# Kernel optimization log

Hardware: AMD Instinct MI355X
Metric: run time of the kernel (lower is better)

The kernel has to match this reference:

```python
import jax, jax.numpy as jnp
import numpy as np

SIZE = 65536
MAX_EDGES = 16777216  # n_edges = min(0.1*SIZE^2, MAX_EDGES) = MAX_EDGES, so all edges active


def setup_inputs() -> dict:
    key = jax.random.key(0)
    k1, k2, k3, k4 = jax.random.split(key, 4)
    x = jax.random.normal(k1, (SIZE,), dtype=jnp.float32)
    edge_weights = jax.random.normal(k2, (MAX_EDGES,), dtype=jnp.float32) * (2.0 / SIZE) ** 0.5
    bias = jnp.zeros((SIZE,), dtype=jnp.float32)
    src = jax.random.randint(k3, (MAX_EDGES,), 0, SIZE, dtype=jnp.int64 if jax.config.jax_enable_x64 else jnp.int32)
    dst = jax.random.randint(k4, (MAX_EDGES,), 0, SIZE, dtype=jnp.int64 if jax.config.jax_enable_x64 else jnp.int32)
    return {"x": x, "edge_weights": edge_weights, "bias": bias, "src": src, "dst": dst}


def reference(x, edge_weights, bias, src, dst):
    # gather -> elementwise multiply -> scatter_add -> + bias
    weighted = x[src] * edge_weights                    # [E]
    out = jax.ops.segment_sum(weighted, dst, num_segments=SIZE)  # [size]
    return out + bias
```

## Files before the change

kernel.cpp:

```cpp
#include <hip/hip_runtime.h>


#define NNODES  65536
#define NEDGES  16777216
#define THREADS 1024
#define NCOPIES 128
#define GROUPS  16
#define CPG     (NCOPIES / GROUPS)
#define RANGES  2
#define BINS    (NNODES / RANGES)

#define FIXSCALE   4194304.0f
#define FIXINV     (1.0f / 4194304.0f)

template <bool HALF>
__global__ __launch_bounds__(THREADS, 4) void wx_lds_kernel(
    const float* __restrict__ x,
    const float* __restrict__ w,
    const int*   __restrict__ src,
    void*        __restrict__ wxv)
{
    extern __shared__ _Float16 xs[];

    for (int i = threadIdx.x; i < NNODES / 4; i += THREADS) {
        float4 v = ((const float4*)x)[i];
        union { _Float16 hh[4]; short4 s4; } u;
        u.hh[0] = (_Float16)v.x; u.hh[1] = (_Float16)v.y;
        u.hh[2] = (_Float16)v.z; u.hh[3] = (_Float16)v.w;
        ((short4*)xs)[i] = u.s4;
    }
    __syncthreads();

    const int n8 = NEDGES / 8;
    const int gs = gridDim.x * THREADS;
    for (int i = blockIdx.x * THREADS + (int)threadIdx.x; i < n8; i += gs) {
        int4   s0 = ((const int4*)src)[2 * i];
        int4   s1 = ((const int4*)src)[2 * i + 1];
        float4 w0 = ((const float4*)w)[2 * i];
        float4 w1 = ((const float4*)w)[2 * i + 1];

        float v[8] = {
            (float)xs[s0.x] * w0.x, (float)xs[s0.y] * w0.y,
            (float)xs[s0.z] * w0.z, (float)xs[s0.w] * w0.w,
            (float)xs[s1.x] * w1.x, (float)xs[s1.y] * w1.y,
            (float)xs[s1.z] * w1.z, (float)xs[s1.w] * w1.w };

        if constexpr (HALF) {
            union { _Float16 hh[8]; int4 p; } u;
            #pragma unroll
            for (int k = 0; k < 8; ++k) u.hh[k] = (_Float16)v[k];
            ((int4*)wxv)[i] = u.p;
        } else {
            float4 o0 = { v[0], v[1], v[2], v[3] };
            float4 o1 = { v[4], v[5], v[6], v[7] };
            ((float4*)wxv)[2 * i]     = o0;
            ((float4*)wxv)[2 * i + 1] = o1;
        }
    }
}

template <bool HALF>
__global__ __launch_bounds__(THREADS, 4) void hist2_kernel(
    const int*  __restrict__ dst,
    const void* __restrict__ wxv,
    float*      __restrict__ ws,
    int B)
{
    extern __shared__ int hi[];

    const int b = blockIdx.x;
    int r, c;
    if (B == NCOPIES) {
        r = (b >> 3) & (RANGES - 1);
        c = (b & 7) | ((b >> 4) << 3);
    } else {
        r = b & (RANGES - 1);
        c = b >> 1;
    }
    const int lo = r * BINS;

    for (int i = threadIdx.x; i < BINS; i += THREADS) hi[i] = 0;
    __syncthreads();

    const int4* dst4 = (const int4*)dst;
    const int n8     = NEDGES / 8;
    const int stride = B * THREADS;
    int g = c * THREADS + (int)threadIdx.x;

    if ((n8 % (2 * stride)) == 0 && n8 >= 2 * stride) {
        const int niter2 = n8 / (2 * stride);
        for (int it = 0; it < niter2; ++it, g += 2 * stride) {
            const int ga = g;
            const int gb = g + stride;

            int4 dA0 = dst4[2 * ga], dA1 = dst4[2 * ga + 1];
            int4 dB0 = dst4[2 * gb], dB1 = dst4[2 * gb + 1];

            float vv[16];
            if constexpr (HALF) {
                int4 pa = ((const int4*)wxv)[ga];
                int4 pb = ((const int4*)wxv)[gb];
                union { int4 p; _Float16 hh[8]; } ua, ub;
                ua.p = pa; ub.p = pb;
                #pragma unroll
                for (int k = 0; k < 8; ++k) {
                    vv[k]     = (float)ua.hh[k];
                    vv[8 + k] = (float)ub.hh[k];
                }
            } else {
                const float4* wx4 = (const float4*)wxv;
                float4 wA0 = wx4[2 * ga], wA1 = wx4[2 * ga + 1];
                float4 wB0 = wx4[2 * gb], wB1 = wx4[2 * gb + 1];
                vv[0]=wA0.x;  vv[1]=wA0.y;  vv[2]=wA0.z;  vv[3]=wA0.w;
                vv[4]=wA1.x;  vv[5]=wA1.y;  vv[6]=wA1.z;  vv[7]=wA1.w;
                vv[8]=wB0.x;  vv[9]=wB0.y;  vv[10]=wB0.z; vv[11]=wB0.w;
                vv[12]=wB1.x; vv[13]=wB1.y; vv[14]=wB1.z; vv[15]=wB1.w;
            }

            unsigned bin[16] = {
                (unsigned)(dA0.x - lo), (unsigned)(dA0.y - lo),
                (unsigned)(dA0.z - lo), (unsigned)(dA0.w - lo),
                (unsigned)(dA1.x - lo), (unsigned)(dA1.y - lo),
                (unsigned)(dA1.z - lo), (unsigned)(dA1.w - lo),
                (unsigned)(dB0.x - lo), (unsigned)(dB0.y - lo),
                (unsigned)(dB0.z - lo), (unsigned)(dB0.w - lo),
                (unsigned)(dB1.x - lo), (unsigned)(dB1.y - lo),
                (unsigned)(dB1.z - lo), (unsigned)(dB1.w - lo) };

            #pragma unroll
            for (int k = 0; k < 16; ++k) {
                if (bin[k] < (unsigned)BINS) {
                    int iv = __float2int_rn(vv[k] * FIXSCALE);
                    atomicAdd(&hi[bin[k]], iv);
                }
            }
        }
    } else {
        for (; g < n8; g += stride) {
            int4 d0 = dst4[2 * g], d1 = dst4[2 * g + 1];
            float vv[8];
            if constexpr (HALF) {
                int4 p = ((const int4*)wxv)[g];
                union { int4 p; _Float16 hh[8]; } u; u.p = p;
                #pragma unroll
                for (int k = 0; k < 8; ++k) vv[k] = (float)u.hh[k];
            } else {
                const float4* wx4 = (const float4*)wxv;
                float4 a = wx4[2 * g], bb = wx4[2 * g + 1];
                vv[0]=a.x; vv[1]=a.y; vv[2]=a.z; vv[3]=a.w;
                vv[4]=bb.x; vv[5]=bb.y; vv[6]=bb.z; vv[7]=bb.w;
            }
            unsigned bin[8] = {
                (unsigned)(d0.x - lo), (unsigned)(d0.y - lo),
                (unsigned)(d0.z - lo), (unsigned)(d0.w - lo),
                (unsigned)(d1.x - lo), (unsigned)(d1.y - lo),
                (unsigned)(d1.z - lo), (unsigned)(d1.w - lo) };
            #pragma unroll
            for (int k = 0; k < 8; ++k) {
                if (bin[k] < (unsigned)BINS) {
                    int iv = __float2int_rn(vv[k] * FIXSCALE);
                    atomicAdd(&hi[bin[k]], iv);
                }
            }
        }
    }
    __syncthreads();

    float* outc = ws + (size_t)c * NNODES + lo;
    for (int i = threadIdx.x; i < BINS; i += THREADS)
        outc[i] = (float)hi[i] * FIXINV;
}

__global__ __launch_bounds__(THREADS, 4) void hist_kernel(
    const float* __restrict__ x,
    const float* __restrict__ w,
    const int*   __restrict__ src,
    const int*   __restrict__ dst,
    float*       __restrict__ ws,
    int B)
{
    extern __shared__ float h[];

    const int b = blockIdx.x;
    int r, c;
    if (B == NCOPIES) {
        r = (b >> 3) & (RANGES - 1);
        c = (b & 7) | ((b >> 4) << 3);
    } else {
        r = b & (RANGES - 1);
        c = b >> 1;
    }
    const int lo = r * BINS;

    for (int i = threadIdx.x; i < BINS; i += THREADS) h[i] = 0.0f;
    __syncthreads();

    const int4*   src4 = (const int4*)src;
    const int4*   dst4 = (const int4*)dst;
    const float4* wgt4 = (const float4*)w;

    const int n8     = NEDGES / 8;
    const int stride = B * THREADS;
    int g = c * THREADS + (int)threadIdx.x;

    if ((n8 % (2 * stride)) == 0 && n8 >= 2 * stride) {
        const int niter2 = n8 / (2 * stride);
        for (int it = 0; it < niter2; ++it, g += 2 * stride) {
            const int ga = g;
            const int gb = g + stride;

            int4   sA0 = src4[2 * ga], sA1 = src4[2 * ga + 1];
            int4   sB0 = src4[2 * gb], sB1 = src4[2 * gb + 1];
            int4   dA0 = dst4[2 * ga], dA1 = dst4[2 * ga + 1];
            int4   dB0 = dst4[2 * gb], dB1 = dst4[2 * gb + 1];
            float4 wA0 = wgt4[2 * ga], wA1 = wgt4[2 * ga + 1];
            float4 wB0 = wgt4[2 * gb], wB1 = wgt4[2 * gb + 1];

            int s[16] = { sA0.x, sA0.y, sA0.z, sA0.w,
                          sA1.x, sA1.y, sA1.z, sA1.w,
                          sB0.x, sB0.y, sB0.z, sB0.w,
                          sB1.x, sB1.y, sB1.z, sB1.w };
            unsigned bin[16] = {
                (unsigned)(dA0.x - lo), (unsigned)(dA0.y - lo),
                (unsigned)(dA0.z - lo), (unsigned)(dA0.w - lo),
                (unsigned)(dA1.x - lo), (unsigned)(dA1.y - lo),
                (unsigned)(dA1.z - lo), (unsigned)(dA1.w - lo),
                (unsigned)(dB0.x - lo), (unsigned)(dB0.y - lo),
                (unsigned)(dB0.z - lo), (unsigned)(dB0.w - lo),
                (unsigned)(dB1.x - lo), (unsigned)(dB1.y - lo),
                (unsigned)(dB1.z - lo), (unsigned)(dB1.w - lo) };
            float wv[16] = { wA0.x, wA0.y, wA0.z, wA0.w,
                             wA1.x, wA1.y, wA1.z, wA1.w,
                             wB0.x, wB0.y, wB0.z, wB0.w,
                             wB1.x, wB1.y, wB1.z, wB1.w };

            float v[16];
            #pragma unroll
            for (int k = 0; k < 16; ++k) {
                v[k] = 0.0f;
                if (bin[k] < (unsigned)BINS) v[k] = x[s[k]] * wv[k];
            }
            #pragma unroll
            for (int k = 0; k < 16; ++k) {
                if (bin[k] < (unsigned)BINS) atomicAdd(&h[bin[k]], v[k]);
            }
        }
    } else {
        for (; g < n8; g += stride) {
            int4   sa = src4[2 * g], sb = src4[2 * g + 1];
            int4   da = dst4[2 * g], db = dst4[2 * g + 1];
            float4 wa = wgt4[2 * g], wb = wgt4[2 * g + 1];

            int      s[8]  = { sa.x, sa.y, sa.z, sa.w, sb.x, sb.y, sb.z, sb.w };
            unsigned bin[8] = {
                (unsigned)(da.x - lo), (unsigned)(da.y - lo),
                (unsigned)(da.z - lo), (unsigned)(da.w - lo),
                (unsigned)(db.x - lo), (unsigned)(db.y - lo),
                (unsigned)(db.z - lo), (unsigned)(db.w - lo) };
            float    wv[8] = { wa.x, wa.y, wa.z, wa.w, wb.x, wb.y, wb.z, wb.w };

            float v[8];
            #pragma unroll
            for (int k = 0; k < 8; ++k) {
                v[k] = 0.0f;
                if (bin[k] < (unsigned)BINS) v[k] = x[s[k]] * wv[k];
            }
            #pragma unroll
            for (int k = 0; k < 8; ++k) {
                if (bin[k] < (unsigned)BINS) atomicAdd(&h[bin[k]], v[k]);
            }
        }
    }
    __syncthreads();

    float* outc = ws + (size_t)c * NNODES + lo;
    for (int i = threadIdx.x; i < BINS; i += THREADS) outc[i] = h[i];
}

__global__ __launch_bounds__(256) void reduceA_kernel(float* __restrict__ ws)
{
    const int NB = NNODES / (256 * 4);
    int g  = blockIdx.x / NB;
    int jb = blockIdx.x % NB;
    int i4 = jb * 256 + (int)threadIdx.x;

    float4* w4 = (float4*)ws;
    const int stride4 = NNODES / 4;

    float4 acc = w4[(size_t)(g * CPG) * stride4 + i4];
    #pragma unroll
    for (int cc = 1; cc < CPG; ++cc) {
        float4 t = w4[(size_t)(g * CPG + cc) * stride4 + i4];
        acc.x += t.x; acc.y += t.y; acc.z += t.z; acc.w += t.w;
    }
    w4[(size_t)(g * CPG) * stride4 + i4] = acc;
}

__global__ __launch_bounds__(256) void reduceB_kernel(
    const float* __restrict__ ws,
    const float* __restrict__ bias,
    float*       __restrict__ out)
{
    int i4 = blockIdx.x * 256 + (int)threadIdx.x;
    const float4* w4 = (const float4*)ws;
    const int stride4 = NNODES / 4;

    float4 acc = ((const float4*)bias)[i4];
    #pragma unroll
    for (int g = 0; g < GROUPS; ++g) {
        float4 t = w4[(size_t)(g * CPG) * stride4 + i4];
        acc.x += t.x; acc.y += t.y; acc.z += t.z; acc.w += t.w;
    }
    ((float4*)out)[i4] = acc;
}

__global__ __launch_bounds__(256) void reduce_generic_kernel(
    const float* __restrict__ ws,
    const float* __restrict__ bias,
    float*       __restrict__ out,
    int B)
{
    int i = blockIdx.x * 256 + (int)threadIdx.x;
    float acc = bias[i];
    for (int cc = 0; cc < B; ++cc) acc += ws[(size_t)cc * NNODES + i];
    out[i] = acc;
}

__global__ __launch_bounds__(256) void init_out_kernel(
    const float* __restrict__ bias, float* __restrict__ out)
{
    int i = blockIdx.x * blockDim.x + threadIdx.x;
    if (i < NNODES) out[i] = bias[i];
}

__global__ __launch_bounds__(256) void edge_atomic_kernel(
    const float* __restrict__ x, const float* __restrict__ w,
    const int* __restrict__ src, const int* __restrict__ dst,
    float* __restrict__ out)
{
    const int n4 = NEDGES / 4;
    int tid = blockIdx.x * blockDim.x + threadIdx.x;
    int stride = gridDim.x * blockDim.x;
    for (int i = tid; i < n4; i += stride) {
        int4 s = ((const int4*)src)[i];
        int4 d = ((const int4*)dst)[i];
        float4 ww = ((const float4*)w)[i];
        atomicAdd(&out[d.x], x[s.x] * ww.x);
        atomicAdd(&out[d.y], x[s.y] * ww.y);
        atomicAdd(&out[d.z], x[s.z] * ww.z);
        atomicAdd(&out[d.w], x[s.w] * ww.w);
    }
}

extern "C" void kernel_launch(void* const* d_in, const int* in_sizes, int n_in,
                              void* d_out, int out_size, void* d_ws, size_t ws_size,
                              hipStream_t stream) {
    const float* x    = (const float*)d_in[0];
    const float* w    = (const float*)d_in[1];
    const float* bias = (const float*)d_in[2];
    const int*   src  = (const int*)d_in[3];
    const int*   dst  = (const int*)d_in[4];
    float* out = (float*)d_out;
    float* ws  = (float*)d_ws;

    const size_t copiesBytes = (size_t)NCOPIES * NNODES * sizeof(float);
    const size_t xLds = (size_t)NNODES * sizeof(_Float16);

    if (ws_size >= copiesBytes + (size_t)NEDGES * sizeof(float)) {
        void* wx = (void*)((char*)d_ws + copiesBytes);
        wx_lds_kernel<false><<<256, THREADS, xLds, stream>>>(x, w, src, wx);
        hist2_kernel<false><<<NCOPIES * RANGES, THREADS,
                              BINS * sizeof(int), stream>>>(dst, wx, ws, NCOPIES);
        reduceA_kernel<<<GROUPS * (NNODES / 1024), 256, 0, stream>>>(ws);
        reduceB_kernel<<<NNODES / 1024, 256, 0, stream>>>(ws, bias, out);
    } else if (ws_size >= copiesBytes + (size_t)NEDGES * 2) {
        void* wx = (void*)((char*)d_ws + copiesBytes);
        wx_lds_kernel<true><<<256, THREADS, xLds, stream>>>(x, w, src, wx);
        hist2_kernel<true><<<NCOPIES * RANGES, THREADS,
                             BINS * sizeof(int), stream>>>(dst, wx, ws, NCOPIES);
        reduceA_kernel<<<GROUPS * (NNODES / 1024), 256, 0, stream>>>(ws);
        reduceB_kernel<<<NNODES / 1024, 256, 0, stream>>>(ws, bias, out);
    } else {
        size_t copies = ws_size / ((size_t)NNODES * sizeof(float));
        int B = (int)(copies < NCOPIES ? copies : NCOPIES);
        if (B >= 1) {
            hist_kernel<<<B * RANGES, THREADS, BINS * sizeof(float), stream>>>(
                x, w, src, dst, ws, B);
            if (B == NCOPIES) {
                reduceA_kernel<<<GROUPS * (NNODES / 1024), 256, 0, stream>>>(ws);
                reduceB_kernel<<<NNODES / 1024, 256, 0, stream>>>(ws, bias, out);
            } else {
                reduce_generic_kernel<<<NNODES / 256, 256, 0, stream>>>(ws, bias, out, B);
            }
        } else {
            init_out_kernel<<<NNODES / 256, 256, 0, stream>>>(bias, out);
            edge_atomic_kernel<<<4096, 256, 0, stream>>>(x, w, src, dst, out);
        }
    }
}
```

Before: 243.5 us.

## Always use half-precision intermediate products and software-prefetch edge loads in gather kernel

The launcher now always takes the fp16 path for the intermediate weighted-edge buffer, dropping the fp32 path even when workspace allows it. This halves that buffer's write and read traffic between the gather and histogram kernels. The gather kernel gains a register double-buffered loop that loads the next iteration's src and weight vectors before computing the current one. The fallback hist kernel loses its two-at-a-time unrolled loop for a plain loop. Rounding each product to fp16 adds precision error to the accumulated sums.

New measurement: 230.6 us. -5.3%, faster.

```diff
diff --git a/kernel.cpp b/kernel.cpp
--- a/kernel.cpp
+++ b/kernel.cpp
@@ -31,30 +31,82 @@
     }
     __syncthreads();
 
+    const int4*   src4 = (const int4*)src;
+    const float4* wgt4 = (const float4*)w;
+
     const int n8 = NEDGES / 8;
     const int gs = gridDim.x * THREADS;
-    for (int i = blockIdx.x * THREADS + (int)threadIdx.x; i < n8; i += gs) {
-        int4   s0 = ((const int4*)src)[2 * i];
-        int4   s1 = ((const int4*)src)[2 * i + 1];
-        float4 w0 = ((const float4*)w)[2 * i];
-        float4 w1 = ((const float4*)w)[2 * i + 1];
-
-        float v[8] = {
-            (float)xs[s0.x] * w0.x, (float)xs[s0.y] * w0.y,
-            (float)xs[s0.z] * w0.z, (float)xs[s0.w] * w0.w,
-            (float)xs[s1.x] * w1.x, (float)xs[s1.y] * w1.y,
-            (float)xs[s1.z] * w1.z, (float)xs[s1.w] * w1.w };
-
-        if constexpr (HALF) {
-            union { _Float16 hh[8]; int4 p; } u;
-            #pragma unroll
-            for (int k = 0; k < 8; ++k) u.hh[k] = (_Float16)v[k];
-            ((int4*)wxv)[i] = u.p;
-        } else {
-            float4 o0 = { v[0], v[1], v[2], v[3] };
-            float4 o1 = { v[4], v[5], v[6], v[7] };
-            ((float4*)wxv)[2 * i]     = o0;
-            ((float4*)wxv)[2 * i + 1] = o1;
+    int i = blockIdx.x * THREADS + (int)threadIdx.x;
+
+    if ((n8 % gs) == 0 && (n8 / gs) >= 2) {
+        const int niter = n8 / gs;
+        int4   s0 = src4[2 * i],  s1 = src4[2 * i + 1];
+        float4 w0 = wgt4[2 * i],  w1 = wgt4[2 * i + 1];
+
+        for (int it = 0; it < niter - 1; ++it) {
+            const int inext = i + gs;
+            int4   ns0 = src4[2 * inext], ns1 = src4[2 * inext + 1];
+            float4 nw0 = wgt4[2 * inext], nw1 = wgt4[2 * inext + 1];
+
+            float v[8] = {
+                (float)xs[s0.x] * w0.x, (float)xs[s0.y] * w0.y,
+                (float)xs[s0.z] * w0.z, (float)xs[s0.w] * w0.w,
+                (float)xs[s1.x] * w1.x, (float)xs[s1.y] * w1.y,
+                (float)xs[s1.z] * w1.z, (float)xs[s1.w] * w1.w };
+
+            if constexpr (HALF) {
+                union { _Float16 hh[8]; int4 p; } u;
+                #pragma unroll
+                for (int k = 0; k < 8; ++k) u.hh[k] = (_Float16)v[k];
+                ((int4*)wxv)[i] = u.p;
+            } else {
+                float4 o0 = { v[0], v[1], v[2], v[3] };
+                float4 o1 = { v[4], v[5], v[6], v[7] };
+                ((float4*)wxv)[2 * i]     = o0;
+                ((float4*)wxv)[2 * i + 1] = o1;
+            }
+
+            s0 = ns0; s1 = ns1; w0 = nw0; w1 = nw1;
+            i = inext;
+        }
+        {
+            float v[8] = {
+                (float)xs[s0.x] * w0.x, (float)xs[s0.y] * w0.y,
+                (float)xs[s0.z] * w0.z, (float)xs[s0.w] * w0.w,
+                (float)xs[s1.x] * w1.x, (float)xs[s1.y] * w1.y,
+                (float)xs[s1.z] * w1.z, (float)xs[s1.w] * w1.w };
+            if constexpr (HALF) {
+                union { _Float16 hh[8]; int4 p; } u;
+                #pragma unroll
+                for (int k = 0; k < 8; ++k) u.hh[k] = (_Float16)v[k];
+                ((int4*)wxv)[i] = u.p;
+            } else {
+                float4 o0 = { v[0], v[1], v[2], v[3] };
+                float4 o1 = { v[4], v[5], v[6], v[7] };
+                ((float4*)wxv)[2 * i]     = o0;
+                ((float4*)wxv)[2 * i + 1] = o1;
+            }
+        }
+    } else {
+        for (; i < n8; i += gs) {
+            int4   s0 = src4[2 * i], s1 = src4[2 * i + 1];
+            float4 w0 = wgt4[2 * i], w1 = wgt4[2 * i + 1];
+            float v[8] = {
+                (float)xs[s0.x] * w0.x, (float)xs[s0.y] * w0.y,
+                (float)xs[s0.z] * w0.z, (float)xs[s0.w] * w0.w,
+                (float)xs[s1.x] * w1.x, (float)xs[s1.y] * w1.y,
+                (float)xs[s1.z] * w1.z, (float)xs[s1.w] * w1.w };
+            if constexpr (HALF) {
+                union { _Float16 hh[8]; int4 p; } u;
+                #pragma unroll
+                for (int k = 0; k < 8; ++k) u.hh[k] = (_Float16)v[k];
+                ((int4*)wxv)[i] = u.p;
+            } else {
+                float4 o0 = { v[0], v[1], v[2], v[3] };
+                float4 o1 = { v[4], v[5], v[6], v[7] };
+                ((float4*)wxv)[2 * i]     = o0;
+                ((float4*)wxv)[2 * i + 1] = o1;
+            }
         }
     }
 }
@@ -203,72 +255,28 @@
     const int stride = B * THREADS;
     int g = c * THREADS + (int)threadIdx.x;
 
-    if ((n8 % (2 * stride)) == 0 && n8 >= 2 * stride) {
-        const int niter2 = n8 / (2 * stride);
-        for (int it = 0; it < niter2; ++it, g += 2 * stride) {
-            const int ga = g;
-            const int gb = g + stride;
-
-            int4   sA0 = src4[2 * ga], sA1 = src4[2 * ga + 1];
-            int4   sB0 = src4[2 * gb], sB1 = src4[2 * gb + 1];
-            int4   dA0 = dst4[2 * ga], dA1 = dst4[2 * ga + 1];
-            int4   dB0 = dst4[2 * gb], dB1 = dst4[2 * gb + 1];
-            float4 wA0 = wgt4[2 * ga], wA1 = wgt4[2 * ga + 1];
-            float4 wB0 = wgt4[2 * gb], wB1 = wgt4[2 * gb + 1];
-
-            int s[16] = { sA0.x, sA0.y, sA0.z, sA0.w,
-                          sA1.x, sA1.y, sA1.z, sA1.w,
-                          sB0.x, sB0.y, sB0.z, sB0.w,
-                          sB1.x, sB1.y, sB1.z, sB1.w };
-            unsigned bin[16] = {
-                (unsigned)(dA0.x - lo), (unsigned)(dA0.y - lo),
-                (unsigned)(dA0.z - lo), (unsigned)(dA0.w - lo),
-                (unsigned)(dA1.x - lo), (unsigned)(dA1.y - lo),
-                (unsigned)(dA1.z - lo), (unsigned)(dA1.w - lo),
-                (unsigned)(dB0.x - lo), (unsigned)(dB0.y - lo),
-                (unsigned)(dB0.z - lo), (unsigned)(dB0.w - lo),
-                (unsigned)(dB1.x - lo), (unsigned)(dB1.y - lo),
-                (unsigned)(dB1.z - lo), (unsigned)(dB1.w - lo) };
-            float wv[16] = { wA0.x, wA0.y, wA0.z, wA0.w,
-                             wA1.x, wA1.y, wA1.z, wA1.w,
-                             wB0.x, wB0.y, wB0.z, wB0.w,
-                             wB1.x, wB1.y, wB1.z, wB1.w };
-
-            float v[16];
-            #pragma unroll
-            for (int k = 0; k < 16; ++k) {
-                v[k] = 0.0f;
-                if (bin[k] < (unsigned)BINS) v[k] = x[s[k]] * wv[k];
-            }
-            #pragma unroll
-            for (int k = 0; k < 16; ++k) {
-                if (bin[k] < (unsigned)BINS) atomicAdd(&h[bin[k]], v[k]);
-            }
-        }
-    } else {
-        for (; g < n8; g += stride) {
-            int4   sa = src4[2 * g], sb = src4[2 * g + 1];
-            int4   da = dst4[2 * g], db = dst4[2 * g + 1];
-            float4 wa = wgt4[2 * g], wb = wgt4[2 * g + 1];
-
-            int      s[8]  = { sa.x, sa.y, sa.z, sa.w, sb.x, sb.y, sb.z, sb.w };
-            unsigned bin[8] = {
-                (unsigned)(da.x - lo), (unsigned)(da.y - lo),
-                (unsigned)(da.z - lo), (unsigned)(da.w - lo),
-                (unsigned)(db.x - lo), (unsigned)(db.y - lo),
-                (unsigned)(db.z - lo), (unsigned)(db.w - lo) };
-            float    wv[8] = { wa.x, wa.y, wa.z, wa.w, wb.x, wb.y, wb.z, wb.w };
-
-            float v[8];
-            #pragma unroll
-            for (int k = 0; k < 8; ++k) {
-                v[k] = 0.0f;
-                if (bin[k] < (unsigned)BINS) v[k] = x[s[k]] * wv[k];
-            }
-            #pragma unroll
-            for (int k = 0; k < 8; ++k) {
-                if (bin[k] < (unsigned)BINS) atomicAdd(&h[bin[k]], v[k]);
-            }
+    for (; g < n8; g += stride) {
+        int4   sa = src4[2 * g], sb = src4[2 * g + 1];
+        int4   da = dst4[2 * g], db = dst4[2 * g + 1];
+        float4 wa = wgt4[2 * g], wb = wgt4[2 * g + 1];
+
+        int      s[8]  = { sa.x, sa.y, sa.z, sa.w, sb.x, sb.y, sb.z, sb.w };
+        unsigned bin[8] = {
+            (unsigned)(da.x - lo), (unsigned)(da.y - lo),
+            (unsigned)(da.z - lo), (unsigned)(da.w - lo),
+            (unsigned)(db.x - lo), (unsigned)(db.y - lo),
+            (unsigned)(db.z - lo), (unsigned)(db.w - lo) };
+        float    wv[8] = { wa.x, wa.y, wa.z, wa.w, wb.x, wb.y, wb.z, wb.w };
+
+        float v[8];
+        #pragma unroll
+        for (int k = 0; k < 8; ++k) {
+            v[k] = 0.0f;
+            if (bin[k] < (unsigned)BINS) v[k] = x[s[k]] * wv[k];
+        }
+        #pragma unroll
+        for (int k = 0; k < 8; ++k) {
+            if (bin[k] < (unsigned)BINS) atomicAdd(&h[bin[k]], v[k]);
         }
     }
     __syncthreads();
@@ -366,14 +374,7 @@
     const size_t copiesBytes = (size_t)NCOPIES * NNODES * sizeof(float);
     const size_t xLds = (size_t)NNODES * sizeof(_Float16);
 
-    if (ws_size >= copiesBytes + (size_t)NEDGES * sizeof(float)) {
-        void* wx = (void*)((char*)d_ws + copiesBytes);
-        wx_lds_kernel<false><<<256, THREADS, xLds, stream>>>(x, w, src, wx);
-        hist2_kernel<false><<<NCOPIES * RANGES, THREADS,
-                              BINS * sizeof(int), stream>>>(dst, wx, ws, NCOPIES);
-        reduceA_kernel<<<GROUPS * (NNODES / 1024), 256, 0, stream>>>(ws);
-        reduceB_kernel<<<NNODES / 1024, 256, 0, stream>>>(ws, bias, out);
-    } else if (ws_size >= copiesBytes + (size_t)NEDGES * 2) {
+    if (ws_size >= copiesBytes + (size_t)NEDGES * 2) {
         void* wx = (void*)((char*)d_ws + copiesBytes);
         wx_lds_kernel<true><<<256, THREADS, xLds, stream>>>(x, w, src, wx);
         hist2_kernel<true><<<NCOPIES * RANGES, THREADS,
```
